# Performance work log

Hardware: AMD Instinct MI355X
Metric: run time of the kernel (lower is better)

Reference implementation:

```python
import jax, jax.numpy as jnp
import numpy as np
from jax import lax


def _max_pool(x, w):
    # x: (B, C, D, H, W); w: 3-tuple spatial window; stride 1, SAME via k//2 pad.
    window = (1, 1) + w
    pads = [(0, 0), (0, 0)] + [(k // 2, k // 2) for k in w]
    return lax.reduce_window(x, -jnp.inf, lax.max, window, (1,) * 5, pads)


def _min_pool(x, w):
    # torch max_pool pads with -inf, so min_pool = -max_pool(-x) exactly.
    return -_max_pool(-x, w)


def soft_skeletonize(x, thresh_width=5):
    for _ in range(thresh_width):
        p1 = _min_pool(x, (3, 1, 1))
        p2 = _min_pool(x, (1, 3, 1))
        p3 = _min_pool(x, (1, 1, 3))
        min_pool_x = jnp.minimum(jnp.minimum(p1, p2), p3)
        contour = jax.nn.relu(_max_pool(min_pool_x, (3, 3, 3)) - min_pool_x)
        x = jax.nn.relu(x - contour)
    return x


def positive_intersection(center_line, vessel):
    clf = center_line.reshape(center_line.shape[0], center_line.shape[1], -1)
    vf = vessel.reshape(vessel.shape[0], vessel.shape[1], -1)
    intersection = (clf * vf).sum(-1)          # (B, C)
    return (intersection.sum(0) + 1e-12) / (clf.sum(-1).sum(0) + 1e-12)  # (C,)


def setup_inputs() -> dict:
    key = jax.random.key(0)
    k1, k2 = jax.random.split(key)
    shape = (2, 1, 192, 192, 192)
    pred = jax.random.uniform(k1, shape, dtype=jnp.float32)
    target = jax.random.uniform(k2, shape, dtype=jnp.float32)
    return {"pred": pred, "target": target}


def reference(pred, target):
    target_skeleton = soft_skeletonize(target)
    cl_pred = soft_skeletonize(pred)
    clrecall = positive_intersection(target_skeleton, pred)[0]
    clacc = positive_intersection(cl_pred, target)[0]
    cldice = 2.0 * clrecall * clacc / (clrecall + clacc)
    return 1.0 - cldice
```

## Files before the change

### kernel.cpp

```cpp
#include <hip/hip_runtime.h>
#include <cfloat>


constexpr int D = 192, H = 192, W = 192, B = 2;
constexpr int HW = H * W;
constexpr int VOL = D * HW;
constexpr int CZ = 12;
constexpr int NCH = D / CZ;
constexpr int WPB = 4;
constexpr int NGY = H / WPB;
constexpr int STEPS = 15;
constexpr int NPART = B * NCH * H;
constexpr int DUMPSZ = 192;

struct F3 { float x, y, z; };

typedef __attribute__((address_space(3))) float lds_f;
typedef __attribute__((address_space(1))) const float glb_f;

__device__ __forceinline__ float min3f(float a, float b, float c) {
  return fminf(fminf(a, b), c);
}
__device__ __forceinline__ float max3f(float a, float b, float c) {
  return fmaxf(fmaxf(a, b), c);
}

__global__ __launch_bounds__(256, 4) void skel_iter(
    const float* __restrict__ srcA, float* __restrict__ dstA,
    const float* __restrict__ othA, double* __restrict__ partA,
    const float* __restrict__ srcB, float* __restrict__ dstB,
    const float* __restrict__ othB, double* __restrict__ partB,
    float* __restrict__ dump, int last) {
  __shared__ float slab[3][8][192];

  const int tid = threadIdx.x, lane = tid & 63, wv = tid >> 6;
  const int bid0 = blockIdx.x + gridDim.x * (blockIdx.y + gridDim.y * blockIdx.z);
  const int nwg = gridDim.x * gridDim.y * gridDim.z;
  const int wid = (bid0 & 7) * (nwg >> 3) + (bid0 >> 3);
  const int gyg = wid % NGY;
  const int combo = wid / NGY;
  const int chunk = combo % NCH;
  const int bz = combo / NCH;
  const int b = bz % B;
  const int chain = bz / B;

  const int gy0 = gyg * WPB;
  const int gy = gy0 + wv;

  const float* __restrict__ vs = (chain ? srcB : srcA) + (size_t)b * VOL;
  float* __restrict__ vd = (chain ? dstB : dstA) + (size_t)b * VOL;
  const float* __restrict__ vo = (chain ? othB : othA) + (size_t)b * VOL;
  double* __restrict__ part = chain ? partB : partA;

  const int z0 = chunk * CZ;
  const int c0 = 3 * lane;
  const int wrow = gy * W + c0;
  float* __restrict__ dmp = dump + c0;

  int roff[5];
  #pragma unroll
  for (int r = 0; r < 5; ++r) {
    const int i = min(max(gy - 2 + r, 0), H - 1) - (gy0 - 2);
    roff[r] = i * 192 + c0;
  }
  const bool ytop = (gy == 0), ybot = (gy == H - 1);
  const bool l0 = (lane == 0), l63 = (lane == 63);

  const int g0 = min(max(gy0 - 2 + wv, 0), H - 1);
  const int g1 = min(max(gy0 + 2 + wv, 0), H - 1);

  auto stage = [&](int plane, int slot) {
    const int zc = min(max(plane, 0), D - 1);
    const float* s0 = vs + (size_t)zc * HW + (size_t)g0 * W + c0;
    const float* s1 = vs + (size_t)zc * HW + (size_t)g1 * W + c0;
    __builtin_amdgcn_global_load_lds((glb_f*)s0, (lds_f*)&slab[slot][wv][0], 12, 0, 0);
    __builtin_amdgcn_global_load_lds((glb_f*)s1, (lds_f*)&slab[slot][wv + 4][0], 12, 0, 0);
  };

  float xa[3][5][3];
  float Mprev[3] = {0, 0, 0}, h1[3] = {0, 0, 0}, h2[3] = {0, 0, 0};
  float sp = 0.0f, ss = 0.0f;

  stage(z0 - 3, 0);
  stage(z0 - 2, 1);
  asm volatile("s_waitcnt vmcnt(0)" ::: "memory");
  __builtin_amdgcn_s_barrier();
  __builtin_amdgcn_sched_barrier(0);
  {
    const float* sp0 = &slab[0][0][0];
    const float* sp1 = &slab[1][0][0];
    #pragma unroll
    for (int r = 1; r <= 3; ++r) {
      const F3 v = *(const F3*)(sp0 + roff[r]);
      xa[1][r][0] = v.x; xa[1][r][1] = v.y; xa[1][r][2] = v.z;
    }
    #pragma unroll
    for (int r = 0; r < 5; ++r) {
      const F3 v = *(const F3*)(sp1 + roff[r]);
      xa[2][r][0] = v.x; xa[2][r][1] = v.y; xa[2][r][2] = v.z;
    }
  }
  xa[1][0][0] = xa[1][0][1] = xa[1][0][2] = 0.0f;
  xa[1][4][0] = xa[1][4][1] = xa[1][4][2] = 0.0f;
  stage(z0 - 1, 2);
  *(F3*)dmp = {0.0f, 0.0f, 0.0f};
  asm volatile("s_waitcnt lgkmcnt(0)" ::: "memory");
  __builtin_amdgcn_s_barrier();
  __builtin_amdgcn_sched_barrier(0);

  #pragma unroll 1
  for (int s3 = 0; s3 < STEPS; s3 += 3) {
    #pragma unroll
    for (int p = 0; p < 3; ++p) {
      const int s = s3 + p;
      const int z = z0 - 1 + s;
      const int zo = z - 2;
      const bool emit = (s >= 3);
      const int NEW = p, OLD = (p + 1) % 3, MID = (p + 2) % 3;
      const int RS = (p + 2) % 3;

      float w0 = 0.f, w1 = 0.f, w2 = 0.f;
      if (last) {
        const F3 wv3 = *(const F3*)(emit ? (vo + (size_t)zo * HW + wrow) : (vo + wrow));
        w0 = wv3.x; w1 = wv3.y; w2 = wv3.z;
      }
      stage(z + 1, p);
      if (last) asm volatile("s_waitcnt vmcnt(4) lgkmcnt(0)" ::: "memory");
      else      asm volatile("s_waitcnt vmcnt(3) lgkmcnt(0)" ::: "memory");
      __builtin_amdgcn_s_barrier();
      __builtin_amdgcn_sched_barrier(0);

      {
        const float* rp = &slab[RS][0][0];
        #pragma unroll
        for (int r = 0; r < 5; ++r) {
          const F3 v = *(const F3*)(rp + roff[r]);
          xa[NEW][r][0] = v.x; xa[NEW][r][1] = v.y; xa[NEW][r][2] = v.z;
        }
      }

      float xl[3], xr[3];
      #pragma unroll
      for (int r = 0; r < 3; ++r) {
        xl[r] = __shfl_up(xa[MID][r + 1][2], 1, 64);
        xr[r] = __shfl_down(xa[MID][r + 1][0], 1, 64);
        if (l0) xl[r] = FLT_MAX;
        if (l63) xr[r] = FLT_MAX;
      }
      float Mc[3][3];
      #pragma unroll
      for (int r = 0; r < 3; ++r) {
        #pragma unroll
        for (int c = 0; c < 3; ++c) {
          const float le = (c == 0) ? xl[r] : xa[MID][r + 1][c - 1];
          const float ri = (c == 2) ? xr[r] : xa[MID][r + 1][c + 1];
          float v = min3f(xa[MID][r + 1][c], le, ri);
          v = min3f(v, xa[MID][r][c], xa[MID][r + 2][c]);
          v = min3f(v, xa[OLD][r + 1][c], xa[NEW][r + 1][c]);
          Mc[r][c] = v;
        }
      }
      if (ytop) { Mc[0][0] = Mc[0][1] = Mc[0][2] = -FLT_MAX; }
      if (ybot) { Mc[2][0] = Mc[2][1] = Mc[2][2] = -FLT_MAX; }

      float rm[3];
      #pragma unroll
      for (int c = 0; c < 3; ++c) rm[c] = max3f(Mc[0][c], Mc[1][c], Mc[2][c]);
      float ml = __shfl_up(rm[2], 1, 64);
      float mr = __shfl_down(rm[0], 1, 64);
      if (l0) ml = -FLT_MAX;
      if (l63) mr = -FLT_MAX;
      float h0c[3];
      h0c[0] = max3f(ml, rm[0], rm[1]);
      h0c[1] = max3f(rm[0], rm[1], rm[2]);
      h0c[2] = max3f(rm[1], rm[2], mr);

      {
        const bool zlo = (zo > 0), zhi = (zo < D - 1);
        float o[3];
        #pragma unroll
        for (int c = 0; c < 3; ++c) {
          float P = h1[c];
          if (zlo) P = fmaxf(P, h2[c]);
          if (zhi) P = fmaxf(P, h0c[c]);
          const float contour = fmaxf(P - Mprev[c], 0.0f);
          o[c] = fmaxf(xa[OLD][2][c] - contour, 0.0f);
        }
        float* dst = (!last && emit) ? (vd + (size_t)zo * HW + wrow) : dmp;
        *(F3*)dst = {o[0], o[1], o[2]};
        if (last && emit) {
          sp += o[0] * w0 + o[1] * w1 + o[2] * w2;
          ss += o[0] + o[1] + o[2];
        }
      }
      #pragma unroll
      for (int c = 0; c < 3; ++c) {
        h2[c] = h1[c]; h1[c] = h0c[c]; Mprev[c] = Mc[1][c];
      }
    }
  }

  if (last) {
    #pragma unroll
    for (int off = 32; off > 0; off >>= 1) {
      sp += __shfl_down(sp, off, 64);
      ss += __shfl_down(ss, off, 64);
    }
    if (lane == 0) {
      const int lin = (b * NCH + chunk) * H + gy;
      part[2 * lin] = (double)sp;
      part[2 * lin + 1] = (double)ss;
    }
  }
}

__global__ void finalize_kernel(const double* __restrict__ pa,
                                const double* __restrict__ pb,
                                float* __restrict__ out, int npart) {
  __shared__ double red[4][4];
  double s[4] = {0, 0, 0, 0};
  for (int i = threadIdx.x; i < npart; i += 256) {
    s[0] += pa[2 * i];
    s[1] += pa[2 * i + 1];
    s[2] += pb[2 * i];
    s[3] += pb[2 * i + 1];
  }
  #pragma unroll
  for (int off = 32; off > 0; off >>= 1)
    #pragma unroll
    for (int j = 0; j < 4; ++j) s[j] += __shfl_down(s[j], off, 64);
  const int wave = threadIdx.x >> 6, lane = threadIdx.x & 63;
  if (lane == 0)
    for (int j = 0; j < 4; ++j) red[j][wave] = s[j];
  __syncthreads();
  if (threadIdx.x == 0) {
    double t[4];
    for (int j = 0; j < 4; ++j)
      t[j] = red[j][0] + red[j][1] + red[j][2] + red[j][3];
    const double recall = (t[0] + 1e-12) / (t[1] + 1e-12);
    const double accv = (t[2] + 1e-12) / (t[3] + 1e-12);
    const double cldice = 2.0 * recall * accv / (recall + accv);
    out[0] = (float)(1.0 - cldice);
  }
}

extern "C" void kernel_launch(void* const* d_in, const int* in_sizes, int n_in,
                              void* d_out, int out_size, void* d_ws, size_t ws_size,
                              hipStream_t stream) {
  const float* pred = (const float*)d_in[0];
  const float* target = (const float*)d_in[1];
  float* out = (float*)d_out;
  const size_t NT = (size_t)VOL * B;

  const dim3 blk(256, 1, 1);
  const size_t need_merged =
      4 * NT * sizeof(float) + 4 * NPART * sizeof(double) + DUMPSZ * sizeof(float);

  if (ws_size >= need_merged) {
    float* a0 = (float*)d_ws;
    float* a1 = a0 + NT;
    float* c0 = a1 + NT;
    float* c1 = c0 + NT;
    double* pA = (double*)(c1 + NT);
    double* pB = pA + 2 * NPART;
    float* dump = (float*)(pB + 2 * NPART);
    const dim3 grd(NGY, NCH, 2 * B);
    skel_iter<<<grd, blk, 0, stream>>>(target, a0, pred, pA, pred, c0, target, pB, dump, 0);
    skel_iter<<<grd, blk, 0, stream>>>(a0, a1, pred, pA, c0, c1, target, pB, dump, 0);
    skel_iter<<<grd, blk, 0, stream>>>(a1, a0, pred, pA, c1, c0, target, pB, dump, 0);
    skel_iter<<<grd, blk, 0, stream>>>(a0, a1, pred, pA, c0, c1, target, pB, dump, 0);
    skel_iter<<<grd, blk, 0, stream>>>(a1, a0, pred, pA, c1, c0, target, pB, dump, 1);
    finalize_kernel<<<1, 256, 0, stream>>>(pA, pB, out, NPART);
  } else {
    float* b0 = (float*)d_ws;
    float* b1 = b0 + NT;
    double* pA = (double*)(b1 + NT);
    double* pB = pA + 2 * NPART;
    float* dump = (float*)(pB + 2 * NPART);
    const dim3 grd(NGY, NCH, B);
    skel_iter<<<grd, blk, 0, stream>>>(target, b0, pred, pA, nullptr, nullptr, nullptr, nullptr, dump, 0);
    skel_iter<<<grd, blk, 0, stream>>>(b0, b1, pred, pA, nullptr, nullptr, nullptr, nullptr, dump, 0);
    skel_iter<<<grd, blk, 0, stream>>>(b1, b0, pred, pA, nullptr, nullptr, nullptr, nullptr, dump, 0);
    skel_iter<<<grd, blk, 0, stream>>>(b0, b1, pred, pA, nullptr, nullptr, nullptr, nullptr, dump, 0);
    skel_iter<<<grd, blk, 0, stream>>>(b1, b0, pred, pA, nullptr, nullptr, nullptr, nullptr, dump, 1);
    skel_iter<<<grd, blk, 0, stream>>>(pred, b0, target, pB, nullptr, nullptr, nullptr, nullptr, dump, 0);
    skel_iter<<<grd, blk, 0, stream>>>(b0, b1, target, pB, nullptr, nullptr, nullptr, nullptr, dump, 0);
    skel_iter<<<grd, blk, 0, stream>>>(b1, b0, target, pB, nullptr, nullptr, nullptr, nullptr, dump, 0);
    skel_iter<<<grd, blk, 0, stream>>>(b0, b1, target, pB, nullptr, nullptr, nullptr, nullptr, dump, 0);
    skel_iter<<<grd, blk, 0, stream>>>(b1, b0, target, pB, nullptr, nullptr, nullptr, nullptr, dump, 1);
    finalize_kernel<<<1, 256, 0, stream>>>(pA, pB, out, NPART);
  }
}
```

Measured before the change: 392.6 us.

## Compute two output rows per wavefront to share vertical halo loads

Each wavefront now produces two adjacent y rows instead of one, so a block covers 8 rows with a 12-row LDS slab instead of 4 rows with an 8-row slab. This cuts the halo overhead in LDS staging (12 loaded rows for 8 outputs instead of 8 for 4) and lets the middle rows' min-pool results be reused for both outputs. The cost is more registers per thread and half as many blocks, which may lower occupancy and parallelism.

```diff
diff --git a/kernel.cpp b/kernel.cpp
--- a/kernel.cpp
+++ b/kernel.cpp
@@ -7,11 +7,11 @@
 constexpr int VOL = D * HW;
 constexpr int CZ = 12;
 constexpr int NCH = D / CZ;
-constexpr int WPB = 4;
-constexpr int NGY = H / WPB;
+constexpr int RPB = 8;
+constexpr int NGY = H / RPB;
 constexpr int STEPS = 15;
-constexpr int NPART = B * NCH * H;
-constexpr int DUMPSZ = 192;
+constexpr int NPART = B * NCH * NGY * 4;
+constexpr int DUMPSZ = 384;
 
 struct F3 { float x, y, z; };
 
@@ -31,7 +31,7 @@
     const float* __restrict__ srcB, float* __restrict__ dstB,
     const float* __restrict__ othB, double* __restrict__ partB,
     float* __restrict__ dump, int last) {
-  __shared__ float slab[3][8][192];
+  __shared__ float slab[3][12][192];
 
   const int tid = threadIdx.x, lane = tid & 63, wv = tid >> 6;
   const int bid0 = blockIdx.x + gridDim.x * (blockIdx.y + gridDim.y * blockIdx.z);
@@ -44,8 +44,8 @@
   const int b = bz % B;
   const int chain = bz / B;
 
-  const int gy0 = gyg * WPB;
-  const int gy = gy0 + wv;
+  const int gy0 = gyg * RPB;
+  const int a = gy0 + 2 * wv;
 
   const float* __restrict__ vs = (chain ? srcB : srcA) + (size_t)b * VOL;
   float* __restrict__ vd = (chain ? dstB : dstA) + (size_t)b * VOL;
@@ -54,31 +54,33 @@
 
   const int z0 = chunk * CZ;
   const int c0 = 3 * lane;
-  const int wrow = gy * W + c0;
+  const int wrowA = a * W + c0;
+  const int wrowB = wrowA + W;
   float* __restrict__ dmp = dump + c0;
-
-  int roff[5];
+  float* __restrict__ dmp2 = dump + 192 + c0;
+
+  const bool ytop = (a == 0), ybot = (a + 1 == H - 1);
+  const bool l0 = (lane == 0), l63 = (lane == 63);
+
+  int g[3];
   #pragma unroll
-  for (int r = 0; r < 5; ++r) {
-    const int i = min(max(gy - 2 + r, 0), H - 1) - (gy0 - 2);
-    roff[r] = i * 192 + c0;
-  }
-  const bool ytop = (gy == 0), ybot = (gy == H - 1);
-  const bool l0 = (lane == 0), l63 = (lane == 63);
-
-  const int g0 = min(max(gy0 - 2 + wv, 0), H - 1);
-  const int g1 = min(max(gy0 + 2 + wv, 0), H - 1);
+  for (int j = 0; j < 3; ++j)
+    g[j] = min(max(gy0 - 2 + wv + 4 * j, 0), H - 1);
 
   auto stage = [&](int plane, int slot) {
     const int zc = min(max(plane, 0), D - 1);
-    const float* s0 = vs + (size_t)zc * HW + (size_t)g0 * W + c0;
-    const float* s1 = vs + (size_t)zc * HW + (size_t)g1 * W + c0;
-    __builtin_amdgcn_global_load_lds((glb_f*)s0, (lds_f*)&slab[slot][wv][0], 12, 0, 0);
-    __builtin_amdgcn_global_load_lds((glb_f*)s1, (lds_f*)&slab[slot][wv + 4][0], 12, 0, 0);
+    const float* base = vs + (size_t)zc * HW;
+    __builtin_amdgcn_global_load_lds((glb_f*)(base + (size_t)g[0] * W + c0),
+                                     (lds_f*)&slab[slot][wv][0], 12, 0, 0);
+    __builtin_amdgcn_global_load_lds((glb_f*)(base + (size_t)g[1] * W + c0),
+                                     (lds_f*)&slab[slot][wv + 4][0], 12, 0, 0);
+    __builtin_amdgcn_global_load_lds((glb_f*)(base + (size_t)g[2] * W + c0),
+                                     (lds_f*)&slab[slot][wv + 8][0], 12, 0, 0);
   };
 
-  float xa[3][5][3];
-  float Mprev[3] = {0, 0, 0}, h1[3] = {0, 0, 0}, h2[3] = {0, 0, 0};
+  float xa[3][6][3];
+  float MprevA[3] = {0, 0, 0}, h1A[3] = {0, 0, 0}, h2A[3] = {0, 0, 0};
+  float MprevB[3] = {0, 0, 0}, h1B[3] = {0, 0, 0}, h2B[3] = {0, 0, 0};
   float sp = 0.0f, ss = 0.0f;
 
   stage(z0 - 3, 0);
@@ -87,23 +89,24 @@
   __builtin_amdgcn_s_barrier();
   __builtin_amdgcn_sched_barrier(0);
   {
-    const float* sp0 = &slab[0][0][0];
-    const float* sp1 = &slab[1][0][0];
-    #pragma unroll
-    for (int r = 1; r <= 3; ++r) {
-      const F3 v = *(const F3*)(sp0 + roff[r]);
+    const float* s0 = &slab[0][2 * wv][0];
+    const float* s1 = &slab[1][2 * wv][0];
+    #pragma unroll
+    for (int r = 1; r <= 4; ++r) {
+      const F3 v = *(const F3*)(s0 + r * 192 + c0);
       xa[1][r][0] = v.x; xa[1][r][1] = v.y; xa[1][r][2] = v.z;
     }
     #pragma unroll
-    for (int r = 0; r < 5; ++r) {
-      const F3 v = *(const F3*)(sp1 + roff[r]);
+    for (int r = 0; r < 6; ++r) {
+      const F3 v = *(const F3*)(s1 + r * 192 + c0);
       xa[2][r][0] = v.x; xa[2][r][1] = v.y; xa[2][r][2] = v.z;
     }
   }
   xa[1][0][0] = xa[1][0][1] = xa[1][0][2] = 0.0f;
-  xa[1][4][0] = xa[1][4][1] = xa[1][4][2] = 0.0f;
+  xa[1][5][0] = xa[1][5][1] = xa[1][5][2] = 0.0f;
   stage(z0 - 1, 2);
   *(F3*)dmp = {0.0f, 0.0f, 0.0f};
+  *(F3*)dmp2 = {0.0f, 0.0f, 0.0f};
   asm volatile("s_waitcnt lgkmcnt(0)" ::: "memory");
   __builtin_amdgcn_s_barrier();
   __builtin_amdgcn_sched_barrier(0);
@@ -119,37 +122,40 @@
       const int NEW = p, OLD = (p + 1) % 3, MID = (p + 2) % 3;
       const int RS = (p + 2) % 3;
 
-      float w0 = 0.f, w1 = 0.f, w2 = 0.f;
+      float wa0 = 0.f, wa1 = 0.f, wa2 = 0.f, wb0 = 0.f, wb1 = 0.f, wb2 = 0.f;
       if (last) {
-        const F3 wv3 = *(const F3*)(emit ? (vo + (size_t)zo * HW + wrow) : (vo + wrow));
-        w0 = wv3.x; w1 = wv3.y; w2 = wv3.z;
+        const float* wbase = emit ? (vo + (size_t)zo * HW) : vo;
+        const F3 wa = *(const F3*)(wbase + wrowA);
+        const F3 wb = *(const F3*)(wbase + wrowB);
+        wa0 = wa.x; wa1 = wa.y; wa2 = wa.z;
+        wb0 = wb.x; wb1 = wb.y; wb2 = wb.z;
       }
       stage(z + 1, p);
-      if (last) asm volatile("s_waitcnt vmcnt(4) lgkmcnt(0)" ::: "memory");
-      else      asm volatile("s_waitcnt vmcnt(3) lgkmcnt(0)" ::: "memory");
+      if (last) asm volatile("s_waitcnt vmcnt(7) lgkmcnt(0)" ::: "memory");
+      else      asm volatile("s_waitcnt vmcnt(5) lgkmcnt(0)" ::: "memory");
       __builtin_amdgcn_s_barrier();
       __builtin_amdgcn_sched_barrier(0);
 
       {
-        const float* rp = &slab[RS][0][0];
+        const float* rp = &slab[RS][2 * wv][0];
         #pragma unroll
-        for (int r = 0; r < 5; ++r) {
-          const F3 v = *(const F3*)(rp + roff[r]);
+        for (int r = 0; r < 6; ++r) {
+          const F3 v = *(const F3*)(rp + r * 192 + c0);
           xa[NEW][r][0] = v.x; xa[NEW][r][1] = v.y; xa[NEW][r][2] = v.z;
         }
       }
 
-      float xl[3], xr[3];
+      float xl[4], xr[4];
       #pragma unroll
-      for (int r = 0; r < 3; ++r) {
+      for (int r = 0; r < 4; ++r) {
         xl[r] = __shfl_up(xa[MID][r + 1][2], 1, 64);
         xr[r] = __shfl_down(xa[MID][r + 1][0], 1, 64);
         if (l0) xl[r] = FLT_MAX;
         if (l63) xr[r] = FLT_MAX;
       }
-      float Mc[3][3];
+      float Mc[4][3];
       #pragma unroll
-      for (int r = 0; r < 3; ++r) {
+      for (int r = 0; r < 4; ++r) {
         #pragma unroll
         for (int c = 0; c < 3; ++c) {
           const float le = (c == 0) ? xl[r] : xa[MID][r + 1][c - 1];
@@ -161,41 +167,54 @@
         }
       }
       if (ytop) { Mc[0][0] = Mc[0][1] = Mc[0][2] = -FLT_MAX; }
-      if (ybot) { Mc[2][0] = Mc[2][1] = Mc[2][2] = -FLT_MAX; }
-
-      float rm[3];
+      if (ybot) { Mc[3][0] = Mc[3][1] = Mc[3][2] = -FLT_MAX; }
+
+      float vmA[3], vmB[3];
       #pragma unroll
-      for (int c = 0; c < 3; ++c) rm[c] = max3f(Mc[0][c], Mc[1][c], Mc[2][c]);
-      float ml = __shfl_up(rm[2], 1, 64);
-      float mr = __shfl_down(rm[0], 1, 64);
-      if (l0) ml = -FLT_MAX;
-      if (l63) mr = -FLT_MAX;
-      float h0c[3];
-      h0c[0] = max3f(ml, rm[0], rm[1]);
-      h0c[1] = max3f(rm[0], rm[1], rm[2]);
-      h0c[2] = max3f(rm[1], rm[2], mr);
+      for (int c = 0; c < 3; ++c) {
+        vmA[c] = max3f(Mc[0][c], Mc[1][c], Mc[2][c]);
+        vmB[c] = max3f(Mc[1][c], Mc[2][c], Mc[3][c]);
+      }
+      float mlA = __shfl_up(vmA[2], 1, 64), mrA = __shfl_down(vmA[0], 1, 64);
+      float mlB = __shfl_up(vmB[2], 1, 64), mrB = __shfl_down(vmB[0], 1, 64);
+      if (l0) { mlA = -FLT_MAX; mlB = -FLT_MAX; }
+      if (l63) { mrA = -FLT_MAX; mrB = -FLT_MAX; }
+      float h0A[3], h0B[3];
+      h0A[0] = max3f(mlA, vmA[0], vmA[1]);
+      h0A[1] = max3f(vmA[0], vmA[1], vmA[2]);
+      h0A[2] = max3f(vmA[1], vmA[2], mrA);
+      h0B[0] = max3f(mlB, vmB[0], vmB[1]);
+      h0B[1] = max3f(vmB[0], vmB[1], vmB[2]);
+      h0B[2] = max3f(vmB[1], vmB[2], mrB);
 
       {
         const bool zlo = (zo > 0), zhi = (zo < D - 1);
-        float o[3];
+        float oA[3], oB[3];
         #pragma unroll
         for (int c = 0; c < 3; ++c) {
-          float P = h1[c];
-          if (zlo) P = fmaxf(P, h2[c]);
-          if (zhi) P = fmaxf(P, h0c[c]);
-          const float contour = fmaxf(P - Mprev[c], 0.0f);
-          o[c] = fmaxf(xa[OLD][2][c] - contour, 0.0f);
-        }
-        float* dst = (!last && emit) ? (vd + (size_t)zo * HW + wrow) : dmp;
-        *(F3*)dst = {o[0], o[1], o[2]};
+          float PA = h1A[c], PB = h1B[c];
+          if (zlo) { PA = fmaxf(PA, h2A[c]); PB = fmaxf(PB, h2B[c]); }
+          if (zhi) { PA = fmaxf(PA, h0A[c]); PB = fmaxf(PB, h0B[c]); }
+          oA[c] = fmaxf(xa[OLD][2][c] - fmaxf(PA - MprevA[c], 0.0f), 0.0f);
+          oB[c] = fmaxf(xa[OLD][3][c] - fmaxf(PB - MprevB[c], 0.0f), 0.0f);
+        }
+        if (!last && emit) {
+          *(F3*)(vd + (size_t)zo * HW + wrowA) = {oA[0], oA[1], oA[2]};
+          *(F3*)(vd + (size_t)zo * HW + wrowB) = {oB[0], oB[1], oB[2]};
+        } else {
+          *(F3*)dmp = {oA[0], oA[1], oA[2]};
+          *(F3*)dmp2 = {oB[0], oB[1], oB[2]};
+        }
         if (last && emit) {
-          sp += o[0] * w0 + o[1] * w1 + o[2] * w2;
-          ss += o[0] + o[1] + o[2];
+          sp += oA[0] * wa0 + oA[1] * wa1 + oA[2] * wa2
+              + oB[0] * wb0 + oB[1] * wb1 + oB[2] * wb2;
+          ss += oA[0] + oA[1] + oA[2] + oB[0] + oB[1] + oB[2];
         }
       }
       #pragma unroll
       for (int c = 0; c < 3; ++c) {
-        h2[c] = h1[c]; h1[c] = h0c[c]; Mprev[c] = Mc[1][c];
+        h2A[c] = h1A[c]; h1A[c] = h0A[c]; MprevA[c] = Mc[1][c];
+        h2B[c] = h1B[c]; h1B[c] = h0B[c]; MprevB[c] = Mc[2][c];
       }
     }
   }
@@ -207,7 +226,7 @@
       ss += __shfl_down(ss, off, 64);
     }
     if (lane == 0) {
-      const int lin = (b * NCH + chunk) * H + gy;
+      const int lin = ((b * NCH + chunk) * NGY + gyg) * 4 + wv;
       part[2 * lin] = (double)sp;
       part[2 * lin + 1] = (double)ss;
     }
```

New measurement: 377.3 us. -3.9%, faster.
